# Performance work log

Hardware: AMD Instinct MI355X
Metric: run time of the kernel (lower is better)

Reference implementation:

```python
import jax, jax.numpy as jnp
import numpy as np
import math

# Spherical conv per Esteves et al. spherical CNNs (sph_conv_batch):
#   1) spherical-harmonic transform of input on an n x n equiangular grid
#   2) per-degree multiply by zonal filter coeffs w[c_in, l, c_out],
#      scaled by 2*pi*sqrt(4*pi/(2l+1))
#   3) inverse transform, plus bias add.
# Implemented as FFT over longitude + Legendre quadrature over colatitude.

BATCH, N_GRID, C_IN, C_OUT = 64, 32, 128, 128
L_MAX = N_GRID // 2  # spherical-harmonic bandwidth


def _legendre_Q(L, n):
    """Normalized associated Legendre N_lm * P_l^m(cos theta_j).
    Returns Q (L, 2L-1, n) with m index offset by L-1, and theta (n,)."""
    theta = np.pi * (np.arange(n) + 0.5) / n
    x, sx = np.cos(theta), np.sin(theta)
    P = np.zeros((L, L, n))
    P[0, 0] = 1.0
    for m in range(1, L):
        P[m, m] = -(2 * m - 1) * sx * P[m - 1, m - 1]
    for m in range(L - 1):
        P[m + 1, m] = (2 * m + 1) * x * P[m, m]
        for l in range(m + 2, L):
            P[l, m] = ((2 * l - 1) * x * P[l - 1, m] - (l + m - 1) * P[l - 2, m]) / (l - m)
    Q = np.zeros((L, 2 * L - 1, n))
    for l in range(L):
        for m in range(l + 1):
            Nlm = np.sqrt((2 * l + 1) / (4 * np.pi)
                          * np.exp(math.lgamma(l - m + 1) - math.lgamma(l + m + 1)))
            Q[l, L - 1 + m] = Nlm * P[l, m]
            Q[l, L - 1 - m] = ((-1) ** m) * Nlm * P[l, m]
    return Q, theta


def _sph_conv(inputs, weights, bias):
    b, n, _, c_in = inputs.shape
    L = weights.shape[1]
    Q, theta = _legendre_Q(L, n)
    # quadrature: sin(theta)*dtheta*dphi, dtheta = pi/n, dphi = 2*pi/n
    wj = np.sin(theta) * (np.pi / n) * (2.0 * np.pi / n)
    Qw = jnp.asarray(Q * wj, dtype=jnp.float32).astype(jnp.complex64)   # (L, 2L-1, n)
    Qs = jnp.asarray(Q, dtype=jnp.float32).astype(jnp.complex64)
    ms = np.arange(-(L - 1), L) % n  # 2L-1 distinct FFT bins
    # forward SHT: FFT over phi then Legendre quadrature over theta
    F = jnp.fft.fft(inputs.astype(jnp.complex64), axis=2)[:, :, ms, :]  # (b, n, 2L-1, c_in)
    coef = jnp.einsum('lmj,bjmc->blmc', Qw, F)                          # (b, L, 2L-1, c_in)
    # zonal spectral filter: per-degree scale 2*pi*sqrt(4*pi/(2l+1))
    scale = jnp.asarray(2.0 * np.pi * np.sqrt(4.0 * np.pi / (2.0 * np.arange(L) + 1.0)),
                        jnp.float32)
    chat = jnp.einsum('blmi,ilo->blmo', coef, weights.astype(jnp.complex64))
    chat = chat * scale[None, :, None, None]
    # inverse SHT: Legendre synthesis then inverse FFT over phi
    G = jnp.einsum('blmo,lmj->bjmo', chat, Qs)                          # (b, n, 2L-1, c_out)
    Gfull = jnp.zeros((b, n, n, G.shape[-1]), jnp.complex64).at[:, :, ms, :].set(G)
    out = jnp.real(jnp.fft.ifft(Gfull, axis=2)) * n                    # (b, n, n, c_out)
    return out + bias


def setup_inputs() -> dict:
    key = jax.random.key(0)
    k1, k2 = jax.random.split(key)
    std = 2.0 / (2.0 * np.pi * np.sqrt(L_MAX * C_IN))
    inputs = jax.random.normal(k1, (BATCH, N_GRID, N_GRID, C_IN), jnp.float32)
    weights = jax.random.normal(k2, (C_IN, L_MAX, C_OUT), jnp.float32) * std
    bias = jnp.zeros((1, 1, 1, C_OUT), jnp.float32)
    return {"inputs": inputs, "weights": weights, "bias": bias}


def reference(inputs, weights, bias):
    return _sph_conv(inputs, weights, bias)
```

## Files before the change

kernel.cpp:

```cpp
#include <hip/hip_runtime.h>
#include <hip/hip_bf16.h>
#include <math.h>


#define NPAIR 136
#define PADC 140
#define WT_OFF (8u << 20)

typedef __attribute__((ext_vector_type(8))) short short8;
typedef __attribute__((ext_vector_type(4))) float f32x4;
#define MFMA16(A, B, C) __builtin_amdgcn_mfma_f32_16x16x32_bf16(A, B, C, 0, 0, 0)

static __device__ __forceinline__ float us2f(unsigned int u) {
  union { unsigned int i; float f; } v; v.i = u << 16; return v.f;
}
static __device__ __forceinline__ unsigned short f2us(float f) {
  __hip_bfloat16 h = __float2bfloat16(f);
  return *(unsigned short*)&h;
}
static __device__ __forceinline__ float lo_f(unsigned int pk) {
  union { unsigned int i; float f; } v; v.i = pk << 16; return v.f;
}
static __device__ __forceinline__ float hi_f(unsigned int pk) {
  union { unsigned int i; float f; } v; v.i = pk & 0xffff0000u; return v.f;
}
static __device__ __forceinline__ unsigned int packbf(float a, float b) {
  return (unsigned int)f2us(a) | ((unsigned int)f2us(b) << 16);
}

__device__ __align__(16) unsigned short g_atab_h[NPAIR * 32];
__device__ __align__(16) float          g_stab[32 * PADC];
__device__ int g_tab_ready;

static __device__ __forceinline__ int detect_fp32(const void* xin) {
  const unsigned short* u = (const unsigned short*)xin;
  int lane = threadIdx.x & 63;
  int big = 0;
#pragma unroll
  for (int q = 0; q < 4; ++q) {
    float v = us2f((unsigned int)u[lane * 8 + q * 2]);
    if (!(fabsf(v) <= 1e3f)) big = 1;
  }
  unsigned long long mask = __ballot(big);
  return (__popcll(mask) >= 16) ? 1 : 0;
}

#define DEF_TRIG \
  constexpr float CT[32] = { \
    1.0f, 0.98078528f, 0.92387953f, 0.83146961f, 0.70710678f, 0.55557023f, \
    0.38268343f, 0.19509032f, 0.0f, -0.19509032f, -0.38268343f, -0.55557023f, \
    -0.70710678f, -0.83146961f, -0.92387953f, -0.98078528f, -1.0f, \
    -0.98078528f, -0.92387953f, -0.83146961f, -0.70710678f, -0.55557023f, \
    -0.38268343f, -0.19509032f, 0.0f, 0.19509032f, 0.38268343f, 0.55557023f, \
    0.70710678f, 0.83146961f, 0.92387953f, 0.98078528f }; \
  constexpr float ST[32] = { \
    0.0f, 0.19509032f, 0.38268343f, 0.55557023f, 0.70710678f, 0.83146961f, \
    0.92387953f, 0.98078528f, 1.0f, 0.98078528f, 0.92387953f, 0.83146961f, \
    0.70710678f, 0.55557023f, 0.38268343f, 0.19509032f, 0.0f, \
    -0.19509032f, -0.38268343f, -0.55557023f, -0.70710678f, -0.83146961f, \
    -0.92387953f, -0.98078528f, -1.0f, -0.98078528f, -0.92387953f, \
    -0.83146961f, -0.70710678f, -0.55557023f, -0.38268343f, -0.19509032f }

__global__ void k_init() {
  if (g_tab_ready) return;
  const int pair = blockIdx.x, j = threadIdx.x;
  int m = 0;
#pragma unroll
  for (int mm = 1; mm < 16; ++mm) {
    int off = mm * 16 - (mm * (mm - 1)) / 2;
    if (off <= pair) m = mm;
  }
  const int l = m + (pair - (m * 16 - (m * (m - 1)) / 2));
  double theta = M_PI * (j + 0.5) / 32.0;
  double x = cos(theta), sx = sin(theta);
  double wj = sx * (M_PI / 32.0) * (2.0 * M_PI / 32.0);
  double pmm = 1.0;
  for (int k = 1; k <= m; ++k) pmm *= -(2.0 * k - 1.0) * sx;
  double p = pmm, pl1 = 0.0, pl2 = 0.0;
  for (int ll = m; ll <= l; ++ll) {
    if (ll == m)          p = pmm;
    else if (ll == m + 1) p = (2.0 * m + 1.0) * x * pmm;
    else                  p = ((2.0 * ll - 1.0) * x * pl1 - (double)(ll + m - 1) * pl2) / (double)(ll - m);
    pl2 = pl1; pl1 = p;
  }
  double r = 1.0;
  for (int k = l - m + 1; k <= l + m; ++k) r *= (double)k;
  double Nlm = sqrt((2.0 * l + 1.0) / (4.0 * M_PI) / r);
  g_atab_h[pair * 32 + j] = f2us((float)(Nlm * p * wj));
  g_stab[j * PADC + pair] = (float)(Nlm * p * (2.0 * M_PI * sqrt(4.0 * M_PI / (2.0 * l + 1.0)))
                                    * (m ? 2.0 : 1.0));
  if (pair == NPAIR - 1 && j == 31) g_tab_ready = 1;
}

__global__ __launch_bounds__(256) void k_fwd(const void* __restrict__ xin,
                                             unsigned int* __restrict__ ws,
                                             const void* __restrict__ Wv) {
  const int fp32m = detect_fp32(xin);
  __shared__ __align__(16) unsigned short xs[32 * 264];
  __shared__ __align__(16) unsigned short fsp2[16 * 16 * 36];
  const int blk = blockIdx.x;
  const int b = (blk & 7) | (((blk >> 7) & 7) << 3);
  const int cq = (blk >> 3) & 15;
  const int t = threadIdx.x;
  uint4 at0 = ((const uint4*)g_atab_h)[t];
  uint4 at1 = ((const uint4*)g_atab_h)[t + 256];
  uint4 at2;
  if (t < 32) at2 = ((const uint4*)g_atab_h)[512 + t];
  if (blk < 512) {
    const int loe = blk * 4 + (t >> 6);
    const int l = loe >> 7, o = loe & 127, c0 = (t & 63) * 2;
    unsigned int pk;
    if (fp32m) {
      const float* Wf = (const float*)Wv;
      pk = packbf(Wf[(size_t)c0 * 2048 + l * 128 + o],
                  Wf[(size_t)(c0 + 1) * 2048 + l * 128 + o]);
    } else {
      const unsigned short* Wh = (const unsigned short*)Wv;
      pk = (unsigned int)Wh[(size_t)c0 * 2048 + l * 128 + o]
         | ((unsigned int)Wh[(size_t)(c0 + 1) * 2048 + l * 128 + o] << 16);
    }
    ((unsigned int*)((char*)ws + WT_OFF))[(size_t)loe * 64 + (c0 >> 1)] = pk;
  }
  if (fp32m) {
    const float* xf = (const float*)xin;
#pragma unroll
    for (int it = 0; it < 8; ++it) {
      int i = t + it * 256;
      int s = i >> 1, hf = i & 1;
      float4 v = *(const float4*)(xf + ((size_t)b * 1024 + s) * 128 + cq * 8 + hf * 4);
      int p = s & 31, j = s >> 5;
      *(uint2*)&xs[p * 264 + j * 8 + hf * 4] = make_uint2(packbf(v.x, v.y), packbf(v.z, v.w));
    }
  } else {
    const unsigned short* xh = (const unsigned short*)xin;
#pragma unroll
    for (int it = 0; it < 4; ++it) {
      int s = t + it * 256;
      uint4 v = *(const uint4*)(xh + ((size_t)b * 1024 + s) * 128 + cq * 8);
      int p = s & 31, j = s >> 5;
      *(uint4*)&xs[p * 264 + j * 8] = v;
    }
  }
  __syncthreads();
  {
    DEF_TRIG;
    const int j = t >> 3, c = t & 7, rb = j * 8 + c;
    float x0  = us2f((unsigned int)xs[rb]);
    float x16 = us2f((unsigned int)xs[16 * 264 + rb]);
    float sp[16], dm[16];
#pragma unroll
    for (int p = 1; p <= 15; ++p) {
      float a  = us2f((unsigned int)xs[p * 264 + rb]);
      float bq = us2f((unsigned int)xs[(32 - p) * 264 + rb]);
      sp[p] = a + bq; dm[p] = a - bq;
    }
#pragma unroll
    for (int mi = 0; mi < 16; ++mi) {
      float re = x0 + ((mi & 1) ? -x16 : x16);
      float im = 0.f;
#pragma unroll
      for (int p = 1; p <= 15; ++p) {
        re += sp[p] * CT[(mi * p) & 31];
        im -= dm[p] * ST[(mi * p) & 31];
      }
      fsp2[(mi * 16 + 2 * c + 0) * 36 + j] = f2us(re);
      fsp2[(mi * 16 + 2 * c + 1) * 36 + j] = f2us(im);
    }
  }
  __syncthreads();
  ((uint4*)xs)[t] = at0;
  ((uint4*)xs)[t + 256] = at1;
  if (t < 32) ((uint4*)xs)[512 + t] = at2;
  __syncthreads();
  {
    const int wv = t >> 6, lane = t & 63;
    const int n = lane & 15, quad = lane >> 4;
    const unsigned short* atab = (const unsigned short*)xs;
#pragma unroll
    for (int mi4 = 0; mi4 < 4; ++mi4) {
      const int mi = wv * 4 + mi4;
      const int base = mi * 16 - (mi * (mi - 1)) / 2;
      short8 A = *(const short8*)&atab[(base + n) * 32 + quad * 8];
      short8 Bv = *(const short8*)&fsp2[(mi * 16 + n) * 36 + quad * 8];
      f32x4 d = {0.f, 0.f, 0.f, 0.f};
      d = MFMA16(A, Bv, d);
#pragma unroll
      for (int reg = 0; reg < 4; ++reg) {
        float other = __shfl_xor(d[reg], 1, 64);
        int slot = quad * 4 + reg;
        if (!(n & 1) && slot < 16 - mi)
          ws[((size_t)b * NPAIR + base + slot) * 128 + cq * 8 + (n >> 1)] =
              packbf(d[reg], other);
      }
    }
  }
}

__global__ __launch_bounds__(1024, 4) void k_cb(const unsigned int* __restrict__ ws,
                                                char* __restrict__ outbuf,
                                                const unsigned short* __restrict__ wt,
                                                const void* __restrict__ biasv,
                                                const void* __restrict__ xin) {
  const int fp32m = detect_fp32(xin);
  __shared__ __align__(16) unsigned int chs[32 * PADC];
  __shared__ __align__(16) float        stb[32 * PADC];
  const int b = blockIdx.x >> 2, oq = blockIdx.x & 3;
  const int t = threadIdx.x;
  for (int i = t; i < 32 * PADC / 4; i += 1024)
    ((float4*)stb)[i] = ((const float4*)g_stab)[i];
  {
    const int lw = t >> 6, lane = t & 63;
    const int col = lane & 15, quad = lane >> 4;
    const int s = col;
    const int av = (s <= lw);
    const int pv = av ? (s * 16 - (s * (s - 1)) / 2 + (lw - s)) : 0;
    short8 Bf[2][4];
#pragma unroll
    for (int nt = 0; nt < 2; ++nt) {
      const unsigned short* wp = wt + ((size_t)lw * 128 + oq * 32 + nt * 16 + col) * 128;
#pragma unroll
      for (int kc = 0; kc < 4; ++kc)
        Bf[nt][kc] = *(const short8*)(wp + kc * 32 + quad * 8);
    }
    f32x4 aR0 = {0.f, 0.f, 0.f, 0.f}, aI0 = aR0, aR1 = aR0, aI1 = aR0;
#pragma unroll
    for (int kc = 0; kc < 4; ++kc) {
      uint4 u0 = {0u, 0u, 0u, 0u}, u1 = u0;
      if (av) {
        const unsigned int* cp = ws + ((size_t)b * NPAIR + pv) * 128 + kc * 32 + quad * 8;
        u0 = *(const uint4*)cp;
        u1 = *(const uint4*)(cp + 4);
      }
      short8 Ar, Ai;
      Ar[0] = (short)(u0.x & 0xffff); Ai[0] = (short)(u0.x >> 16);
      Ar[1] = (short)(u0.y & 0xffff); Ai[1] = (short)(u0.y >> 16);
      Ar[2] = (short)(u0.z & 0xffff); Ai[2] = (short)(u0.z >> 16);
      Ar[3] = (short)(u0.w & 0xffff); Ai[3] = (short)(u0.w >> 16);
      Ar[4] = (short)(u1.x & 0xffff); Ai[4] = (short)(u1.x >> 16);
      Ar[5] = (short)(u1.y & 0xffff); Ai[5] = (short)(u1.y >> 16);
      Ar[6] = (short)(u1.z & 0xffff); Ai[6] = (short)(u1.z >> 16);
      Ar[7] = (short)(u1.w & 0xffff); Ai[7] = (short)(u1.w >> 16);
      aR0 = MFMA16(Ar, Bf[0][kc], aR0);
      aI0 = MFMA16(Ai, Bf[0][kc], aI0);
      aR1 = MFMA16(Ar, Bf[1][kc], aR1);
      aI1 = MFMA16(Ai, Bf[1][kc], aI1);
    }
#pragma unroll
    for (int reg = 0; reg < 4; ++reg) {
      int slot = quad * 4 + reg;
      if (slot <= lw) {
        int pp_ = slot * 16 - (slot * (slot - 1)) / 2 + (lw - slot);
        chs[(0 * 16 + col) * PADC + pp_] = packbf(aR0[reg], aI0[reg]);
        chs[(1 * 16 + col) * PADC + pp_] = packbf(aR1[reg], aI1[reg]);
      }
    }
  }
  const int j = t >> 5, ol = t & 31;
  const int o = oq * 32 + ol;
  const float bv = fp32m ? ((const float*)biasv)[o]
                         : us2f((unsigned int)((const unsigned short*)biasv)[o]);
  __syncthreads();

  float Gr[16], Gi[16];
#pragma unroll
  for (int mm = 0; mm < 16; ++mm) { Gr[mm] = 0.f; Gi[mm] = 0.f; }
  {
    float4 s4 = {0.f, 0.f, 0.f, 0.f};
    uint4  c4 = {0u, 0u, 0u, 0u};
    int pair = 0;
#pragma unroll
    for (int mm = 0; mm < 16; ++mm) {
#pragma unroll
      for (int l = mm; l < 16; ++l) {
        if ((pair & 3) == 0) {
          s4 = *(const float4*)&stb[j * PADC + pair];
          c4 = *(const uint4*)&chs[ol * PADC + pair];
        }
        const int r = pair & 3;
        const float        s  = (r == 0) ? s4.x : (r == 1) ? s4.y : (r == 2) ? s4.z : s4.w;
        const unsigned int cv = (r == 0) ? c4.x : (r == 1) ? c4.y : (r == 2) ? c4.z : c4.w;
        Gr[mm] += s * lo_f(cv);
        Gi[mm] += s * hi_f(cv);
        ++pair;
      }
    }
  }
  DEF_TRIG;
#pragma unroll
  for (int pp = 0; pp <= 16; ++pp) {
    float A = 0.f, Bv = 0.f;
#pragma unroll
    for (int mm = 0; mm < 16; ++mm) {
      A  += Gr[mm] * CT[(mm * pp) & 31];
      Bv += Gi[mm] * ST[(mm * pp) & 31];
    }
    const int p2 = (32 - pp) & 31;
    size_t e1 = (size_t)b * 131072 + (size_t)(j * 32 + pp) * 128 + o;
    size_t e2 = (size_t)b * 131072 + (size_t)(j * 32 + p2) * 128 + o;
    if (fp32m) {
      *(float*)(outbuf + e1 * 4) = bv + A - Bv;
      *(float*)(outbuf + e2 * 4) = bv + A + Bv;
    } else {
      *(unsigned short*)(outbuf + e1 * 2) = f2us(bv + A - Bv);
      *(unsigned short*)(outbuf + e2 * 2) = f2us(bv + A + Bv);
    }
  }
}

extern "C" void kernel_launch(void* const* d_in, const int* in_sizes, int n_in,
                              void* d_out, int out_size, void* d_ws, size_t ws_size,
                              hipStream_t stream) {
  const void* xin  = d_in[0];
  const void* W    = d_in[1];
  const void* bias = d_in[2];
  char* out = (char*)d_out;
  unsigned int* ws = (unsigned int*)d_ws;
  const unsigned short* wt = (const unsigned short*)((char*)d_ws + WT_OFF);

  hipLaunchKernelGGL(k_init, dim3(NPAIR), dim3(32),   0, stream);
  hipLaunchKernelGGL(k_fwd,  dim3(1024),  dim3(256),  0, stream, xin, ws, W);
  hipLaunchKernelGGL(k_cb,   dim3(256),   dim3(1024), 0, stream, ws, out, wt, bias, xin);
}
```

Baseline: 111.0 us.

## Split real/imag coefficient planes and re-grid channel-mix/synthesis kernel into 256-thread blocks

New measurement: 246.3 us. 2.22x slower.

```diff
diff --git a/kernel.cpp b/kernel.cpp
--- a/kernel.cpp
+++ b/kernel.cpp
@@ -5,7 +5,9 @@
 
 #define NPAIR 136
 #define PADC 140
+#define PIM_U (1u << 20)
 #define WT_OFF (8u << 20)
+#define SMEM_BYTES 35328
 
 typedef __attribute__((ext_vector_type(8))) short short8;
 typedef __attribute__((ext_vector_type(4))) float f32x4;
@@ -61,9 +63,7 @@
     -0.92387953f, -0.98078528f, -1.0f, -0.98078528f, -0.92387953f, \
     -0.83146961f, -0.70710678f, -0.55557023f, -0.38268343f, -0.19509032f }
 
-__global__ void k_init() {
-  if (g_tab_ready) return;
-  const int pair = blockIdx.x, j = threadIdx.x;
+static __device__ void tab_compute(int pair, int j) {
   int m = 0;
 #pragma unroll
   for (int mm = 1; mm < 16; ++mm) {
@@ -89,15 +89,21 @@
   g_atab_h[pair * 32 + j] = f2us((float)(Nlm * p * wj));
   g_stab[j * PADC + pair] = (float)(Nlm * p * (2.0 * M_PI * sqrt(4.0 * M_PI / (2.0 * l + 1.0)))
                                     * (m ? 2.0 : 1.0));
-  if (pair == NPAIR - 1 && j == 31) g_tab_ready = 1;
+}
+
+__global__ void k_init() {
+  if (g_tab_ready) return;
+  tab_compute(blockIdx.x, threadIdx.x);
+  if (blockIdx.x == NPAIR - 1 && threadIdx.x == 31) g_tab_ready = 1;
 }
 
 __global__ __launch_bounds__(256) void k_fwd(const void* __restrict__ xin,
                                              unsigned int* __restrict__ ws,
                                              const void* __restrict__ Wv) {
   const int fp32m = detect_fp32(xin);
-  __shared__ __align__(16) unsigned short xs[32 * 264];
-  __shared__ __align__(16) unsigned short fsp2[16 * 16 * 36];
+  __shared__ __align__(16) char smem[SMEM_BYTES];
+  unsigned short* xs   = (unsigned short*)smem;
+  unsigned short* fsp2 = xs + 32 * 264;
   const int blk = blockIdx.x;
   const int b = (blk & 7) | (((blk >> 7) & 7) << 3);
   const int cq = (blk >> 3) & 15;
@@ -186,123 +192,128 @@
       d = MFMA16(A, Bv, d);
 #pragma unroll
       for (int reg = 0; reg < 4; ++reg) {
-        float other = __shfl_xor(d[reg], 1, 64);
+        float other = __shfl_xor(d[reg], 2, 64);
         int slot = quad * 4 + reg;
-        if (!(n & 1) && slot < 16 - mi)
-          ws[((size_t)b * NPAIR + base + slot) * 128 + cq * 8 + (n >> 1)] =
+        int nm = n & 3;
+        if (nm <= 1 && slot < 16 - mi) {
+          unsigned int* plane = ws + (nm ? PIM_U : 0u);
+          plane[((size_t)b * NPAIR + base + slot) * 64 + cq * 4 + (n >> 2)] =
               packbf(d[reg], other);
-      }
-    }
-  }
-}
-
-__global__ __launch_bounds__(1024, 4) void k_cb(const unsigned int* __restrict__ ws,
+        }
+      }
+    }
+  }
+}
+
+__global__ __launch_bounds__(256, 4) void k_cbf(const unsigned int* __restrict__ ws,
                                                 char* __restrict__ outbuf,
-                                                const unsigned short* __restrict__ wt,
                                                 const void* __restrict__ biasv,
                                                 const void* __restrict__ xin) {
   const int fp32m = detect_fp32(xin);
-  __shared__ __align__(16) unsigned int chs[32 * PADC];
-  __shared__ __align__(16) float        stb[32 * PADC];
-  const int b = blockIdx.x >> 2, oq = blockIdx.x & 3;
-  const int t = threadIdx.x;
-  for (int i = t; i < 32 * PADC / 4; i += 1024)
-    ((float4*)stb)[i] = ((const float4*)g_stab)[i];
+  __shared__ __align__(16) char smem[SMEM_BYTES];
+  unsigned int* chs = (unsigned int*)smem;
+  float* stb = (float*)(smem + 32 * PADC * 4);
+  const unsigned short* wt = (const unsigned short*)((const char*)ws + WT_OFF);
+  const int blk = blockIdx.x, t = threadIdx.x;
+  const int b = blk >> 3, oq = (blk >> 1) & 3, jh = blk & 1;
+  for (int i = t; i < 16 * 35; i += 256) {
+    int row = i / 35, w = i % 35;
+    ((float4*)stb)[row * 35 + w] = ((const float4*)g_stab)[(jh * 16 + row) * 35 + w];
+  }
   {
-    const int lw = t >> 6, lane = t & 63;
+    const int wv = t >> 6, lane = t & 63;
     const int col = lane & 15, quad = lane >> 4;
     const int s = col;
-    const int av = (s <= lw);
-    const int pv = av ? (s * 16 - (s * (s - 1)) / 2 + (lw - s)) : 0;
-    short8 Bf[2][4];
-#pragma unroll
-    for (int nt = 0; nt < 2; ++nt) {
-      const unsigned short* wp = wt + ((size_t)lw * 128 + oq * 32 + nt * 16 + col) * 128;
-#pragma unroll
-      for (int kc = 0; kc < 4; ++kc)
-        Bf[nt][kc] = *(const short8*)(wp + kc * 32 + quad * 8);
-    }
-    f32x4 aR0 = {0.f, 0.f, 0.f, 0.f}, aI0 = aR0, aR1 = aR0, aI1 = aR0;
-#pragma unroll
-    for (int kc = 0; kc < 4; ++kc) {
-      uint4 u0 = {0u, 0u, 0u, 0u}, u1 = u0;
-      if (av) {
-        const unsigned int* cp = ws + ((size_t)b * NPAIR + pv) * 128 + kc * 32 + quad * 8;
-        u0 = *(const uint4*)cp;
-        u1 = *(const uint4*)(cp + 4);
-      }
-      short8 Ar, Ai;
-      Ar[0] = (short)(u0.x & 0xffff); Ai[0] = (short)(u0.x >> 16);
-      Ar[1] = (short)(u0.y & 0xffff); Ai[1] = (short)(u0.y >> 16);
-      Ar[2] = (short)(u0.z & 0xffff); Ai[2] = (short)(u0.z >> 16);
-      Ar[3] = (short)(u0.w & 0xffff); Ai[3] = (short)(u0.w >> 16);
-      Ar[4] = (short)(u1.x & 0xffff); Ai[4] = (short)(u1.x >> 16);
-      Ar[5] = (short)(u1.y & 0xffff); Ai[5] = (short)(u1.y >> 16);
-      Ar[6] = (short)(u1.z & 0xffff); Ai[6] = (short)(u1.z >> 16);
-      Ar[7] = (short)(u1.w & 0xffff); Ai[7] = (short)(u1.w >> 16);
-      aR0 = MFMA16(Ar, Bf[0][kc], aR0);
-      aI0 = MFMA16(Ai, Bf[0][kc], aI0);
-      aR1 = MFMA16(Ar, Bf[1][kc], aR1);
-      aI1 = MFMA16(Ai, Bf[1][kc], aI1);
-    }
-#pragma unroll
-    for (int reg = 0; reg < 4; ++reg) {
-      int slot = quad * 4 + reg;
-      if (slot <= lw) {
-        int pp_ = slot * 16 - (slot * (slot - 1)) / 2 + (lw - slot);
-        chs[(0 * 16 + col) * PADC + pp_] = packbf(aR0[reg], aI0[reg]);
-        chs[(1 * 16 + col) * PADC + pp_] = packbf(aR1[reg], aI1[reg]);
-      }
-    }
-  }
-  const int j = t >> 5, ol = t & 31;
+#pragma unroll
+    for (int li = 0; li < 4; ++li) {
+      const int lw = wv * 4 + li;
+      const int av = (s <= lw);
+      const int pv = av ? (s * 16 - (s * (s - 1)) / 2 + (lw - s)) : 0;
+      short8 Bf[2][4];
+#pragma unroll
+      for (int nt = 0; nt < 2; ++nt) {
+        const unsigned short* wp = wt + ((size_t)lw * 128 + oq * 32 + nt * 16 + col) * 128;
+#pragma unroll
+        for (int kc = 0; kc < 4; ++kc)
+          Bf[nt][kc] = *(const short8*)(wp + kc * 32 + quad * 8);
+      }
+      f32x4 aR0 = {0.f, 0.f, 0.f, 0.f}, aI0 = aR0, aR1 = aR0, aI1 = aR0;
+#pragma unroll
+      for (int kc = 0; kc < 4; ++kc) {
+        uint4 ur = {0u, 0u, 0u, 0u}, ui = ur;
+        if (av) {
+          size_t base = ((size_t)b * NPAIR + pv) * 64 + kc * 16 + quad * 4;
+          ur = *(const uint4*)&ws[base];
+          ui = *(const uint4*)&ws[PIM_U + base];
+        }
+        short8 Ar = *(short8*)&ur, Ai = *(short8*)&ui;
+        aR0 = MFMA16(Ar, Bf[0][kc], aR0);
+        aI0 = MFMA16(Ai, Bf[0][kc], aI0);
+        aR1 = MFMA16(Ar, Bf[1][kc], aR1);
+        aI1 = MFMA16(Ai, Bf[1][kc], aI1);
+      }
+#pragma unroll
+      for (int reg = 0; reg < 4; ++reg) {
+        int slot = quad * 4 + reg;
+        if (slot <= lw) {
+          int pp_ = slot * 16 - (slot * (slot - 1)) / 2 + (lw - slot);
+          chs[col * PADC + pp_] = packbf(aR0[reg], aI0[reg]);
+          chs[(16 + col) * PADC + pp_] = packbf(aR1[reg], aI1[reg]);
+        }
+      }
+    }
+  }
+  const int j8 = t >> 5, ol = t & 31;
   const int o = oq * 32 + ol;
   const float bv = fp32m ? ((const float*)biasv)[o]
                          : us2f((unsigned int)((const unsigned short*)biasv)[o]);
   __syncthreads();
-
-  float Gr[16], Gi[16];
-#pragma unroll
-  for (int mm = 0; mm < 16; ++mm) { Gr[mm] = 0.f; Gi[mm] = 0.f; }
-  {
-    float4 s4 = {0.f, 0.f, 0.f, 0.f};
-    uint4  c4 = {0u, 0u, 0u, 0u};
-    int pair = 0;
-#pragma unroll
-    for (int mm = 0; mm < 16; ++mm) {
-#pragma unroll
-      for (int l = mm; l < 16; ++l) {
-        if ((pair & 3) == 0) {
-          s4 = *(const float4*)&stb[j * PADC + pair];
-          c4 = *(const uint4*)&chs[ol * PADC + pair];
+  DEF_TRIG;
+#pragma unroll 1
+  for (int jj = 0; jj < 2; ++jj) {
+    const int jl = j8 * 2 + jj, j = jh * 16 + jl;
+    float Gr[16], Gi[16];
+#pragma unroll
+    for (int mm = 0; mm < 16; ++mm) { Gr[mm] = 0.f; Gi[mm] = 0.f; }
+    {
+      float4 s4 = {0.f, 0.f, 0.f, 0.f};
+      uint4  c4 = {0u, 0u, 0u, 0u};
+      int pair = 0;
+#pragma unroll
+      for (int mm = 0; mm < 16; ++mm) {
+#pragma unroll
+        for (int l = mm; l < 16; ++l) {
+          if ((pair & 3) == 0) {
+            s4 = *(const float4*)&stb[jl * PADC + pair];
+            c4 = *(const uint4*)&chs[ol * PADC + pair];
+          }
+          const int r = pair & 3;
+          const float        s  = (r == 0) ? s4.x : (r == 1) ? s4.y : (r == 2) ? s4.z : s4.w;
+          const unsigned int cv = (r == 0) ? c4.x : (r == 1) ? c4.y : (r == 2) ? c4.z : c4.w;
+          Gr[mm] += s * lo_f(cv);
+          Gi[mm] += s * hi_f(cv);
+          ++pair;
         }
-        const int r = pair & 3;
-        const float        s  = (r == 0) ? s4.x : (r == 1) ? s4.y : (r == 2) ? s4.z : s4.w;
-        const unsigned int cv = (r == 0) ? c4.x : (r == 1) ? c4.y : (r == 2) ? c4.z : c4.w;
-        Gr[mm] += s * lo_f(cv);
-        Gi[mm] += s * hi_f(cv);
-        ++pair;
-      }
-    }
-  }
-  DEF_TRIG;
-#pragma unroll
-  for (int pp = 0; pp <= 16; ++pp) {
-    float A = 0.f, Bv = 0.f;
-#pragma unroll
-    for (int mm = 0; mm < 16; ++mm) {
-      A  += Gr[mm] * CT[(mm * pp) & 31];
-      Bv += Gi[mm] * ST[(mm * pp) & 31];
-    }
-    const int p2 = (32 - pp) & 31;
-    size_t e1 = (size_t)b * 131072 + (size_t)(j * 32 + pp) * 128 + o;
-    size_t e2 = (size_t)b * 131072 + (size_t)(j * 32 + p2) * 128 + o;
-    if (fp32m) {
-      *(float*)(outbuf + e1 * 4) = bv + A - Bv;
-      *(float*)(outbuf + e2 * 4) = bv + A + Bv;
-    } else {
-      *(unsigned short*)(outbuf + e1 * 2) = f2us(bv + A - Bv);
-      *(unsigned short*)(outbuf + e2 * 2) = f2us(bv + A + Bv);
+      }
+    }
+#pragma unroll
+    for (int pp = 0; pp <= 16; ++pp) {
+      float A = 0.f, Bv = 0.f;
+#pragma unroll
+      for (int mm = 0; mm < 16; ++mm) {
+        A  += Gr[mm] * CT[(mm * pp) & 31];
+        Bv += Gi[mm] * ST[(mm * pp) & 31];
+      }
+      const int p2 = (32 - pp) & 31;
+      size_t e1 = (size_t)b * 131072 + (size_t)(j * 32 + pp) * 128 + o;
+      size_t e2 = (size_t)b * 131072 + (size_t)(j * 32 + p2) * 128 + o;
+      if (fp32m) {
+        *(float*)(outbuf + e1 * 4) = bv + A - Bv;
+        *(float*)(outbuf + e2 * 4) = bv + A + Bv;
+      } else {
+        *(unsigned short*)(outbuf + e1 * 2) = f2us(bv + A - Bv);
+        *(unsigned short*)(outbuf + e2 * 2) = f2us(bv + A + Bv);
+      }
     }
   }
 }
@@ -315,9 +326,8 @@
   const void* bias = d_in[2];
   char* out = (char*)d_out;
   unsigned int* ws = (unsigned int*)d_ws;
-  const unsigned short* wt = (const unsigned short*)((char*)d_ws + WT_OFF);
-
-  hipLaunchKernelGGL(k_init, dim3(NPAIR), dim3(32),   0, stream);
-  hipLaunchKernelGGL(k_fwd,  dim3(1024),  dim3(256),  0, stream, xin, ws, W);
-  hipLaunchKernelGGL(k_cb,   dim3(256),   dim3(1024), 0, stream, ws, out, wt, bias, xin);
-}
+
+  hipLaunchKernelGGL(k_init, dim3(NPAIR), dim3(32),  0, stream);
+  hipLaunchKernelGGL(k_fwd,  dim3(1024),  dim3(256), 0, stream, xin, ws, W);
+  hipLaunchKernelGGL(k_cbf,  dim3(512),   dim3(256), 0, stream, ws, out, bias, xin);
+}
```
